# Performance work log

Measured on AMD Instinct MI355X. Metric: run time of the kernel, lower is better.

## Reference

```python
import jax, jax.numpy as jnp
import numpy as np

N_NODES = 50000
IN_CH = 32
HID = 64
N_EDGES = 800000
B = 4


def setup_inputs() -> dict:
    key = jax.random.key(0)
    ks = jax.random.split(key, 20)
    inp = {
        "x": jax.random.normal(ks[0], (B, N_NODES, IN_CH), dtype=jnp.float32),
        "h": jax.random.normal(ks[1], (B, N_NODES, HID), dtype=jnp.float32),
        "edge_index": jax.random.randint(ks[2], (2, N_EDGES), 0, N_NODES, dtype=jnp.int64),
        "edge_weight": jax.random.uniform(ks[3], (N_EDGES,), dtype=jnp.float32),
    }
    # 6 GCNConv layers: uz, hz, ur, hr, uh, hh. W stored as [in, out]; bias [out].
    names = [("uz", IN_CH), ("hz", HID), ("ur", IN_CH), ("hr", HID), ("uh", IN_CH), ("hh", HID)]
    for i, (nm, cin) in enumerate(names):
        scale = 1.0 / np.sqrt(cin)
        inp[f"W_{nm}"] = jax.random.uniform(ks[4 + 2 * i], (cin, HID), minval=-scale, maxval=scale, dtype=jnp.float32)
        inp[f"b_{nm}"] = jax.random.uniform(ks[5 + 2 * i], (HID,), minval=-scale, maxval=scale, dtype=jnp.float32)
    return inp


def _gcn_norm(edge_index, edge_weight, n):
    # add self-loops with weight 1, symmetric normalization (PyG GCNConv default)
    loop = jnp.arange(n, dtype=edge_index.dtype)
    src = jnp.concatenate([edge_index[0], loop])
    dst = jnp.concatenate([edge_index[1], loop])
    w = jnp.concatenate([edge_weight, jnp.ones((n,), edge_weight.dtype)])
    deg = jnp.zeros((n,), edge_weight.dtype).at[dst].add(w)
    dinv = jnp.where(deg > 0, jax.lax.rsqrt(jnp.maximum(deg, 1e-12)), 0.0)
    norm = dinv[src] * w * dinv[dst]
    return src, dst, norm


def _gcn(x, W, b, src, dst, norm, n):
    # x: [B, N, Cin] -> [B, N, H]; linear then normalized scatter-add over edges
    xw = jnp.einsum("bnc,ch->bnh", x, W)
    msg = xw[:, src, :] * norm[None, :, None]          # [B, E+N, H]
    agg = jnp.zeros((x.shape[0], n, W.shape[1]), x.dtype).at[:, dst].add(msg)
    return agg + b


def reference(x, h, edge_index, edge_weight,
              W_uz, b_uz, W_hz, b_hz, W_ur, b_ur, W_hr, b_hr, W_uh, b_uh, W_hh, b_hh):
    n = x.shape[1]
    src, dst, norm = _gcn_norm(edge_index, edge_weight, n)
    z = jax.nn.sigmoid(_gcn(x, W_uz, b_uz, src, dst, norm, n)
                       + _gcn(h, W_hz, b_hz, src, dst, norm, n))
    r = jax.nn.sigmoid(_gcn(x, W_ur, b_ur, src, dst, norm, n)
                       + _gcn(h, W_hr, b_hr, src, dst, norm, n))
    h_hat = jnp.tanh(_gcn(x, W_uh, b_uh, src, dst, norm, n)
                     + _gcn(r * h, W_hh, b_hh, src, dst, norm, n))
    return (1.0 - z) * h + z * h_hat
```

## Files before the change

### kernel.cpp

```cpp
#include <hip/hip_runtime.h>
#include <math.h>

#define NN 50000
#define CIN 32
#define HD  64
#define NE  800000
#define NB  4
#define NBLK 196
#define NTILE 12500
#define TPB   3125

typedef unsigned int uint32;
typedef unsigned short ushort16;
typedef __attribute__((ext_vector_type(8))) short bf16x8;
typedef __attribute__((ext_vector_type(4))) float f32x4;

__device__ __forceinline__ uint32 pk2(float a, float b) {
    uint32 ua = __float_as_uint(a), ub = __float_as_uint(b);
    uint32 ra = (ua + 0x7FFFu + ((ua >> 16) & 1u)) >> 16;
    uint32 rb = (ub + 0x7FFFu + ((ub >> 16) & 1u)) >> 16;
    return ra | (rb << 16);
}
__device__ __forceinline__ ushort16 b1(float v) {
    uint32 u = __float_as_uint(v);
    return (ushort16)((u + 0x7FFFu + ((u >> 16) & 1u)) >> 16);
}
__device__ __forceinline__ float blo(uint32 v) { return __uint_as_float(v << 16); }
__device__ __forceinline__ float bhi(uint32 v) { return __uint_as_float(v & 0xFFFF0000u); }
__device__ __forceinline__ float sigm(float v) { return 1.0f / (1.0f + __expf(-v)); }


__global__ void k_init(float* __restrict__ deg, int* __restrict__ counts) {
    int i = blockIdx.x * blockDim.x + threadIdx.x;
    if (i < NN) { deg[i] = 1.0f; counts[i] = 0; }
}

__global__ void k_deg_count(const int* __restrict__ ei, const float* __restrict__ ew,
                            float* __restrict__ deg, int* __restrict__ counts) {
    int stride = gridDim.x * blockDim.x;
    for (int e = blockIdx.x * blockDim.x + threadIdx.x; e < NE; e += stride) {
        int d = ei[NE + e];
        atomicAdd(&deg[d], ew[e]);
        atomicAdd(&counts[d], 1);
    }
}

__global__ void k_convert(const float* __restrict__ x, const float* __restrict__ h,
                          uint32* __restrict__ F) {
    int stride = gridDim.x * blockDim.x;
    for (int t = blockIdx.x * blockDim.x + threadIdx.x; t < NB * NN * (CIN / 2); t += stride) {
        int cp = t & 15; int rest = t >> 4;
        int b = rest / NN; int n = rest - b * NN;
        float2 v = *(const float2*)&x[(b * NN + n) * CIN + 2 * cp];
        F[n * 192 + b * 16 + cp] = pk2(v.x, v.y);
    }
    for (int t = blockIdx.x * blockDim.x + threadIdx.x; t < NB * NN * (HD / 2); t += stride) {
        int cp = t & 31; int rest = t >> 5;
        int b = rest / NN; int n = rest - b * NN;
        float2 v = *(const float2*)&h[(b * NN + n) * HD + 2 * cp];
        F[n * 192 + 64 + b * 32 + cp] = pk2(v.x, v.y);
    }
}

__global__ void k_pack(const float* __restrict__ Wuz, const float* __restrict__ Whz,
                       const float* __restrict__ Wur, const float* __restrict__ Whr,
                       const float* __restrict__ Wuh, const float* __restrict__ Whh,
                       const float* __restrict__ buz, const float* __restrict__ bhz,
                       const float* __restrict__ bur, const float* __restrict__ bhr,
                       const float* __restrict__ buh, const float* __restrict__ bhh,
                       uint32* __restrict__ WB, float* __restrict__ BS) {
    int t = blockIdx.x * blockDim.x + threadIdx.x;
    if (t < 9216) {
        int g = t / 3072, rem = t - g * 3072;
        int kt = rem >> 10, r2 = rem & 1023;
        int ct = r2 >> 8, r3 = r2 & 255;
        int l = r3 >> 2, jp = r3 & 3;
        int k = kt * 32 + ((l >> 4) << 3) + 2 * jp;
        int ch = ct * 16 + (l & 15);
        const float* Wu = (g == 0) ? Wuz : (g == 1) ? Wur : Wuh;
        const float* Wh = (g == 0) ? Whz : (g == 1) ? Whr : Whh;
        float w0 = (k < 32) ? Wu[k * 64 + ch] : Wh[(k - 32) * 64 + ch];
        int k1 = k + 1;
        float w1 = (k1 < 32) ? Wu[k1 * 64 + ch] : Wh[(k1 - 32) * 64 + ch];
        WB[t] = pk2(w0, w1);
    }
    if (t < 192) {
        int g = t >> 6, c = t & 63;
        const float* bu = (g == 0) ? buz : (g == 1) ? bur : buh;
        const float* bh = (g == 0) ? bhz : (g == 1) ? bhr : bhh;
        BS[t] = bu[c] + bh[c];
    }
}


__global__ void k_scan1(const int* __restrict__ counts, int* __restrict__ tmp,
                        int* __restrict__ partials) {
    __shared__ int lds[256];
    int i = blockIdx.x * 256 + threadIdx.x;
    int v = (i < NN) ? counts[i] : 0;
    lds[threadIdx.x] = v;
    __syncthreads();
    for (int off = 1; off < 256; off <<= 1) {
        int t = (threadIdx.x >= off) ? lds[threadIdx.x - off] : 0;
        __syncthreads();
        lds[threadIdx.x] += t;
        __syncthreads();
    }
    if (i < NN) tmp[i] = lds[threadIdx.x];
    if (threadIdx.x == 255) partials[blockIdx.x] = lds[255];
}

__global__ void k_scan2(int* __restrict__ partials) {
    __shared__ int lds[256];
    int v = (threadIdx.x < NBLK) ? partials[threadIdx.x] : 0;
    lds[threadIdx.x] = v;
    __syncthreads();
    for (int off = 1; off < 256; off <<= 1) {
        int t = (threadIdx.x >= off) ? lds[threadIdx.x - off] : 0;
        __syncthreads();
        lds[threadIdx.x] += t;
        __syncthreads();
    }
    int ex = (threadIdx.x > 0) ? lds[threadIdx.x - 1] : 0;
    if (threadIdx.x < NBLK) partials[threadIdx.x] = ex;
}

__global__ void k_scan3(const int* __restrict__ tmp, const int* __restrict__ counts,
                        const int* __restrict__ partials,
                        int* __restrict__ rowptr, int* __restrict__ cursor,
                        float* __restrict__ deg) {
    int i = blockIdx.x * blockDim.x + threadIdx.x;
    if (i < NN) {
        int inc = tmp[i] + partials[i >> 8];
        rowptr[i + 1] = inc;
        cursor[i] = inc - counts[i];
        if (i == 0) rowptr[0] = 0;
        float dg = deg[i];
        deg[i] = (dg > 0.0f) ? rsqrtf(fmaxf(dg, 1e-12f)) : 0.0f;
    }
}

__global__ void k_bucket(const int* __restrict__ ei, const float* __restrict__ ew,
                         const float* __restrict__ dinv,
                         int* __restrict__ cursor, int2* __restrict__ eb) {
    int stride = gridDim.x * blockDim.x;
    for (int e = blockIdx.x * blockDim.x + threadIdx.x; e < NE; e += stride) {
        int s = ei[e], d = ei[NE + e];
        float nrm = dinv[s] * ew[e] * dinv[d];
        int pos = atomicAdd(&cursor[d], 1);
        eb[pos] = make_int2(s, __float_as_int(nrm));
    }
}


__global__ __launch_bounds__(256) void k_gather_xh(
    const int* __restrict__ rowptr, const int2* __restrict__ eb,
    const float* __restrict__ dinv, const uint32* __restrict__ F,
    uint32* __restrict__ AggU) {

    int l = threadIdx.x & 63;
    int d = __builtin_amdgcn_readfirstlane(blockIdx.x * 4 + (threadIdx.x >> 6));
    float dv = dinv[d];
    float s2 = dv * dv;

    const uint32* fp = F + 3 * l;
    const uint32* sp = fp + d * 192;
    uint32 u0 = sp[0], u1 = sp[1], u2 = sp[2];
    float a0 = s2 * blo(u0), a1 = s2 * bhi(u0);
    float a2 = s2 * blo(u1), a3 = s2 * bhi(u1);
    float a4 = s2 * blo(u2), a5 = s2 * bhi(u2);

    int e  = rowptr[d];
    int e1 = rowptr[d + 1];

    for (; e + 3 < e1; e += 4) {
        int2 p0 = eb[e], p1 = eb[e + 1], p2 = eb[e + 2], p3 = eb[e + 3];
        const uint32* q0 = fp + p0.x * 192;
        const uint32* q1 = fp + p1.x * 192;
        const uint32* q2 = fp + p2.x * 192;
        const uint32* q3 = fp + p3.x * 192;
        uint32 v00 = q0[0], v01 = q0[1], v02 = q0[2];
        uint32 v10 = q1[0], v11 = q1[1], v12 = q1[2];
        uint32 v20 = q2[0], v21 = q2[1], v22 = q2[2];
        uint32 v30 = q3[0], v31 = q3[1], v32 = q3[2];
        float n0 = __int_as_float(p0.y), n1 = __int_as_float(p1.y);
        float n2 = __int_as_float(p2.y), n3 = __int_as_float(p3.y);
        a0 = fmaf(n0, blo(v00), a0); a1 = fmaf(n0, bhi(v00), a1);
        a2 = fmaf(n0, blo(v01), a2); a3 = fmaf(n0, bhi(v01), a3);
        a4 = fmaf(n0, blo(v02), a4); a5 = fmaf(n0, bhi(v02), a5);
        a0 = fmaf(n1, blo(v10), a0); a1 = fmaf(n1, bhi(v10), a1);
        a2 = fmaf(n1, blo(v11), a2); a3 = fmaf(n1, bhi(v11), a3);
        a4 = fmaf(n1, blo(v12), a4); a5 = fmaf(n1, bhi(v12), a5);
        a0 = fmaf(n2, blo(v20), a0); a1 = fmaf(n2, bhi(v20), a1);
        a2 = fmaf(n2, blo(v21), a2); a3 = fmaf(n2, bhi(v21), a3);
        a4 = fmaf(n2, blo(v22), a4); a5 = fmaf(n2, bhi(v22), a5);
        a0 = fmaf(n3, blo(v30), a0); a1 = fmaf(n3, bhi(v30), a1);
        a2 = fmaf(n3, blo(v31), a2); a3 = fmaf(n3, bhi(v31), a3);
        a4 = fmaf(n3, blo(v32), a4); a5 = fmaf(n3, bhi(v32), a5);
    }
    for (; e < e1; ++e) {
        int2 p0 = eb[e];
        const uint32* q0 = fp + p0.x * 192;
        uint32 v00 = q0[0], v01 = q0[1], v02 = q0[2];
        float n0 = __int_as_float(p0.y);
        a0 = fmaf(n0, blo(v00), a0); a1 = fmaf(n0, bhi(v00), a1);
        a2 = fmaf(n0, blo(v01), a2); a3 = fmaf(n0, bhi(v01), a3);
        a4 = fmaf(n0, blo(v02), a4); a5 = fmaf(n0, bhi(v02), a5);
    }

    uint32 w0 = pk2(a0, a1), w1 = pk2(a2, a3), w2 = pk2(a4, a5);
    int j = 3 * l;
    #pragma unroll
    for (int q = 0; q < 3; ++q) {
        uint32 wv = (q == 0) ? w0 : (q == 1) ? w1 : w2;
        int jq = j + q;
        int b, s;
        if (jq < 64) { b = jq >> 4; s = jq & 15; }
        else { int jj = jq - 64; b = jj >> 5; s = 16 + (jj & 31); }
        AggU[(b * NN + d) * 48 + s] = wv;
    }
}

__global__ __launch_bounds__(256) void k_gather_rh(
    const int* __restrict__ rowptr, const int2* __restrict__ eb,
    const float* __restrict__ dinv, const uint32* __restrict__ R,
    uint32* __restrict__ AggU) {

    int l = threadIdx.x & 63;
    int d = __builtin_amdgcn_readfirstlane(blockIdx.x * 4 + (threadIdx.x >> 6));
    float dv = dinv[d];
    float s2 = dv * dv;

    const uint32* rp = R + 2 * l;
    uint2 sv = *(const uint2*)(rp + d * 128);
    float a0 = s2 * blo(sv.x), a1 = s2 * bhi(sv.x);
    float a2 = s2 * blo(sv.y), a3 = s2 * bhi(sv.y);

    int e  = rowptr[d];
    int e1 = rowptr[d + 1];

    for (; e + 3 < e1; e += 4) {
        int2 p0 = eb[e], p1 = eb[e + 1], p2 = eb[e + 2], p3 = eb[e + 3];
        uint2 v0 = *(const uint2*)(rp + p0.x * 128);
        uint2 v1 = *(const uint2*)(rp + p1.x * 128);
        uint2 v2 = *(const uint2*)(rp + p2.x * 128);
        uint2 v3 = *(const uint2*)(rp + p3.x * 128);
        float n0 = __int_as_float(p0.y), n1 = __int_as_float(p1.y);
        float n2 = __int_as_float(p2.y), n3 = __int_as_float(p3.y);
        a0 = fmaf(n0, blo(v0.x), a0); a1 = fmaf(n0, bhi(v0.x), a1);
        a2 = fmaf(n0, blo(v0.y), a2); a3 = fmaf(n0, bhi(v0.y), a3);
        a0 = fmaf(n1, blo(v1.x), a0); a1 = fmaf(n1, bhi(v1.x), a1);
        a2 = fmaf(n1, blo(v1.y), a2); a3 = fmaf(n1, bhi(v1.y), a3);
        a0 = fmaf(n2, blo(v2.x), a0); a1 = fmaf(n2, bhi(v2.x), a1);
        a2 = fmaf(n2, blo(v2.y), a2); a3 = fmaf(n2, bhi(v2.y), a3);
        a0 = fmaf(n3, blo(v3.x), a0); a1 = fmaf(n3, bhi(v3.x), a1);
        a2 = fmaf(n3, blo(v3.y), a2); a3 = fmaf(n3, bhi(v3.y), a3);
    }
    for (; e < e1; ++e) {
        int2 p0 = eb[e];
        uint2 v0 = *(const uint2*)(rp + p0.x * 128);
        float n0 = __int_as_float(p0.y);
        a0 = fmaf(n0, blo(v0.x), a0); a1 = fmaf(n0, bhi(v0.x), a1);
        a2 = fmaf(n0, blo(v0.y), a2); a3 = fmaf(n0, bhi(v0.y), a3);
    }

    int b  = l >> 4;
    int cp = (2 * l) & 31;
    *(uint2*)&AggU[(b * NN + d) * 48 + 16 + cp] = make_uint2(pk2(a0, a1), pk2(a2, a3));
}


__global__ __launch_bounds__(256) void k_zr(
    const uint32* __restrict__ AggU, const float* __restrict__ h,
    const uint32* __restrict__ WB, const float* __restrict__ BS,
    float* __restrict__ z_out, ushort16* __restrict__ R16) {

    int l  = threadIdx.x & 63;
    int t  = blockIdx.x * 4 + (threadIdx.x >> 6);
    int lr = l & 15, lg = l >> 4;

    const bf16x8* wz = (const bf16x8*)WB;
    const bf16x8* wr = (const bf16x8*)(WB + 3072);
    const bf16x8* arow = (const bf16x8*)(AggU + (t * 16 + lr) * 48);
    bf16x8 af0 = arow[0 * 4 + lg];
    bf16x8 af1 = arow[1 * 4 + lg];
    bf16x8 af2 = arow[2 * 4 + lg];

    f32x4 az[4], ar[4];
    #pragma unroll
    for (int c = 0; c < 4; ++c) { az[c] = (f32x4){0,0,0,0}; ar[c] = (f32x4){0,0,0,0}; }

    #pragma unroll
    for (int ct = 0; ct < 4; ++ct) {
        az[ct] = __builtin_amdgcn_mfma_f32_16x16x32_bf16(af0, wz[(0*4+ct)*64 + l], az[ct], 0,0,0);
        ar[ct] = __builtin_amdgcn_mfma_f32_16x16x32_bf16(af0, wr[(0*4+ct)*64 + l], ar[ct], 0,0,0);
        az[ct] = __builtin_amdgcn_mfma_f32_16x16x32_bf16(af1, wz[(1*4+ct)*64 + l], az[ct], 0,0,0);
        ar[ct] = __builtin_amdgcn_mfma_f32_16x16x32_bf16(af1, wr[(1*4+ct)*64 + l], ar[ct], 0,0,0);
        az[ct] = __builtin_amdgcn_mfma_f32_16x16x32_bf16(af2, wz[(2*4+ct)*64 + l], az[ct], 0,0,0);
        ar[ct] = __builtin_amdgcn_mfma_f32_16x16x32_bf16(af2, wr[(2*4+ct)*64 + l], ar[ct], 0,0,0);
    }

    int bb    = t / TPB;
    int pr0   = t * 16;
    int nbase = pr0 - bb * NN;

    #pragma unroll
    for (int ct = 0; ct < 4; ++ct) {
        int ch = ct * 16 + lr;
        float bz = BS[ch];
        float br = BS[64 + ch];
        #pragma unroll
        for (int rr = 0; rr < 4; ++rr) {
            int i    = lg * 4 + rr;
            int off  = (pr0 + i) * 64 + ch;
            float zv = sigm(az[ct][rr] + bz);
            float rv = sigm(ar[ct][rr] + br);
            float hv = h[off];
            z_out[off] = zv;
            R16[(nbase + i) * 256 + bb * 64 + ch] = b1(rv * hv);
        }
    }
}

__global__ __launch_bounds__(256) void k_final(
    const uint32* __restrict__ AggU, const float* __restrict__ h,
    const uint32* __restrict__ WB, const float* __restrict__ BS,
    float* __restrict__ out) {

    int l  = threadIdx.x & 63;
    int t  = blockIdx.x * 4 + (threadIdx.x >> 6);
    int lr = l & 15, lg = l >> 4;

    const bf16x8* wh = (const bf16x8*)(WB + 6144);
    const bf16x8* arow = (const bf16x8*)(AggU + (t * 16 + lr) * 48);
    bf16x8 af0 = arow[0 * 4 + lg];
    bf16x8 af1 = arow[1 * 4 + lg];
    bf16x8 af2 = arow[2 * 4 + lg];

    f32x4 ac[4];
    #pragma unroll
    for (int c = 0; c < 4; ++c) ac[c] = (f32x4){0,0,0,0};

    #pragma unroll
    for (int ct = 0; ct < 4; ++ct) {
        ac[ct] = __builtin_amdgcn_mfma_f32_16x16x32_bf16(af0, wh[(0*4+ct)*64 + l], ac[ct], 0,0,0);
        ac[ct] = __builtin_amdgcn_mfma_f32_16x16x32_bf16(af1, wh[(1*4+ct)*64 + l], ac[ct], 0,0,0);
        ac[ct] = __builtin_amdgcn_mfma_f32_16x16x32_bf16(af2, wh[(2*4+ct)*64 + l], ac[ct], 0,0,0);
    }

    int pr0 = t * 16;

    #pragma unroll
    for (int ct = 0; ct < 4; ++ct) {
        int ch = ct * 16 + lr;
        float bs = BS[128 + ch];
        #pragma unroll
        for (int rr = 0; rr < 4; ++rr) {
            int i   = lg * 4 + rr;
            int off = (pr0 + i) * 64 + ch;
            float hh = tanhf(ac[ct][rr] + bs);
            float zv = out[off];
            float hv = h[off];
            out[off] = (1.0f - zv) * hv + zv * hh;
        }
    }
}


extern "C" void kernel_launch(void* const* d_in, const int* in_sizes, int n_in,
                              void* d_out, int out_size, void* d_ws, size_t ws_size,
                              hipStream_t stream) {
    const float* x   = (const float*)d_in[0];
    const float* h   = (const float*)d_in[1];
    const int*   ei  = (const int*)d_in[2];
    const float* ew  = (const float*)d_in[3];
    const float* Wuz = (const float*)d_in[4];
    const float* buz = (const float*)d_in[5];
    const float* Whz = (const float*)d_in[6];
    const float* bhz = (const float*)d_in[7];
    const float* Wur = (const float*)d_in[8];
    const float* bur = (const float*)d_in[9];
    const float* Whr = (const float*)d_in[10];
    const float* bhr = (const float*)d_in[11];
    const float* Wuh = (const float*)d_in[12];
    const float* buh = (const float*)d_in[13];
    const float* Whh = (const float*)d_in[14];
    const float* bhh = (const float*)d_in[15];
    float* out = (float*)d_out;

    float*  w      = (float*)d_ws;
    float*  dinv   = w;
    int*    rowptr = (int*)(w + 51200);
    int2*   eb     = (int2*)(w + 102400);
    uint32* F      = (uint32*)(w + 1702400);
    uint32* R      = F;
    uint32* AggU   = (uint32*)(w + 11302400);
    uint32* WB     = (uint32*)(w + 20902400);
    float*  BS     = (float*)(w + 20911616);
    int*    counts = (int*)(w + 20911808);
    int*    tmp    = (int*)(w + 20963008);
    int*    cursor = (int*)(w + 21014208);
    int*    parts  = (int*)(w + 21065408);

    k_init<<<(NN + 255) / 256, 256, 0, stream>>>(dinv, counts);
    k_deg_count<<<2048, 256, 0, stream>>>(ei, ew, dinv, counts);
    k_convert<<<2048, 256, 0, stream>>>(x, h, F);
    k_pack<<<36, 256, 0, stream>>>(Wuz, Whz, Wur, Whr, Wuh, Whh,
                                   buz, bhz, bur, bhr, buh, bhh, WB, BS);

    k_scan1<<<NBLK, 256, 0, stream>>>(counts, tmp, parts);
    k_scan2<<<1, 256, 0, stream>>>(parts);
    k_scan3<<<NBLK, 256, 0, stream>>>(tmp, counts, parts, rowptr, cursor, dinv);

    k_bucket<<<2048, 256, 0, stream>>>(ei, ew, dinv, cursor, eb);

    k_gather_xh<<<NN / 4, 256, 0, stream>>>(rowptr, eb, dinv, F, AggU);

    k_zr<<<NTILE / 4, 256, 0, stream>>>(AggU, h, WB, BS, out, (ushort16*)R);

    k_gather_rh<<<NN / 4, 256, 0, stream>>>(rowptr, eb, dinv, R, AggU);

    k_final<<<NTILE / 4, 256, 0, stream>>>(AggU, h, WB, BS, out);
}
```

Baseline: 367.9 us.

## Fuse preprocessing kernels, unroll gathers by 8, persist MFMA weights in registers

Merges degree counting, feature conversion and weight packing into one launch. Both gather kernels get an 8-edge unrolled loop for more loads in flight, and the aggregated buffer switches to a node-major 192-word row layout with contiguous stores. The zr and final kernels become grid-stride over tiles with a fixed wave count and keep their weight fragments and biases in registers. This trades launch and weight-reload cost for higher register pressure and a different store pattern.

Result: slower. 381.7 us (+3.8%).

```diff
diff --git a/kernel.cpp b/kernel.cpp
--- a/kernel.cpp
+++ b/kernel.cpp
@@ -9,9 +9,10 @@
 #define NBLK 196
 #define NTILE 12500
 #define TPB   3125
+#define DWAVES 2048
 
 typedef unsigned int uint32;
-typedef unsigned short ushort16;
+typedef unsigned short ushort_t;
 typedef __attribute__((ext_vector_type(8))) short bf16x8;
 typedef __attribute__((ext_vector_type(4))) float f32x4;
 
@@ -21,9 +22,9 @@
     uint32 rb = (ub + 0x7FFFu + ((ub >> 16) & 1u)) >> 16;
     return ra | (rb << 16);
 }
-__device__ __forceinline__ ushort16 b1(float v) {
+__device__ __forceinline__ ushort_t b1(float v) {
     uint32 u = __float_as_uint(v);
-    return (ushort16)((u + 0x7FFFu + ((u >> 16) & 1u)) >> 16);
+    return (ushort_t)((u + 0x7FFFu + ((u >> 16) & 1u)) >> 16);
 }
 __device__ __forceinline__ float blo(uint32 v) { return __uint_as_float(v << 16); }
 __device__ __forceinline__ float bhi(uint32 v) { return __uint_as_float(v & 0xFFFF0000u); }
@@ -35,43 +36,22 @@
     if (i < NN) { deg[i] = 1.0f; counts[i] = 0; }
 }
 
-__global__ void k_deg_count(const int* __restrict__ ei, const float* __restrict__ ew,
-                            float* __restrict__ deg, int* __restrict__ counts) {
+__global__ void k_pre(const float* __restrict__ x, const float* __restrict__ h,
+                      const int* __restrict__ ei, const float* __restrict__ ew,
+                      const float* __restrict__ Wuz, const float* __restrict__ Whz,
+                      const float* __restrict__ Wur, const float* __restrict__ Whr,
+                      const float* __restrict__ Wuh, const float* __restrict__ Whh,
+                      const float* __restrict__ buz, const float* __restrict__ bhz,
+                      const float* __restrict__ bur, const float* __restrict__ bhr,
+                      const float* __restrict__ buh, const float* __restrict__ bhh,
+                      uint32* __restrict__ F, float* __restrict__ deg,
+                      int* __restrict__ counts,
+                      uint32* __restrict__ WB, float* __restrict__ BS) {
     int stride = gridDim.x * blockDim.x;
-    for (int e = blockIdx.x * blockDim.x + threadIdx.x; e < NE; e += stride) {
-        int d = ei[NE + e];
-        atomicAdd(&deg[d], ew[e]);
-        atomicAdd(&counts[d], 1);
-    }
-}
-
-__global__ void k_convert(const float* __restrict__ x, const float* __restrict__ h,
-                          uint32* __restrict__ F) {
-    int stride = gridDim.x * blockDim.x;
-    for (int t = blockIdx.x * blockDim.x + threadIdx.x; t < NB * NN * (CIN / 2); t += stride) {
-        int cp = t & 15; int rest = t >> 4;
-        int b = rest / NN; int n = rest - b * NN;
-        float2 v = *(const float2*)&x[(b * NN + n) * CIN + 2 * cp];
-        F[n * 192 + b * 16 + cp] = pk2(v.x, v.y);
-    }
-    for (int t = blockIdx.x * blockDim.x + threadIdx.x; t < NB * NN * (HD / 2); t += stride) {
-        int cp = t & 31; int rest = t >> 5;
-        int b = rest / NN; int n = rest - b * NN;
-        float2 v = *(const float2*)&h[(b * NN + n) * HD + 2 * cp];
-        F[n * 192 + 64 + b * 32 + cp] = pk2(v.x, v.y);
-    }
-}
-
-__global__ void k_pack(const float* __restrict__ Wuz, const float* __restrict__ Whz,
-                       const float* __restrict__ Wur, const float* __restrict__ Whr,
-                       const float* __restrict__ Wuh, const float* __restrict__ Whh,
-                       const float* __restrict__ buz, const float* __restrict__ bhz,
-                       const float* __restrict__ bur, const float* __restrict__ bhr,
-                       const float* __restrict__ buh, const float* __restrict__ bhh,
-                       uint32* __restrict__ WB, float* __restrict__ BS) {
-    int t = blockIdx.x * blockDim.x + threadIdx.x;
-    if (t < 9216) {
-        int g = t / 3072, rem = t - g * 3072;
+    int tid = blockIdx.x * blockDim.x + threadIdx.x;
+
+    if (tid < 9216) {
+        int g = tid / 3072, rem = tid - g * 3072;
         int kt = rem >> 10, r2 = rem & 1023;
         int ct = r2 >> 8, r3 = r2 & 255;
         int l = r3 >> 2, jp = r3 & 3;
@@ -82,13 +62,31 @@
         float w0 = (k < 32) ? Wu[k * 64 + ch] : Wh[(k - 32) * 64 + ch];
         int k1 = k + 1;
         float w1 = (k1 < 32) ? Wu[k1 * 64 + ch] : Wh[(k1 - 32) * 64 + ch];
-        WB[t] = pk2(w0, w1);
-    }
-    if (t < 192) {
-        int g = t >> 6, c = t & 63;
+        WB[tid] = pk2(w0, w1);
+    }
+    if (tid < 192) {
+        int g = tid >> 6, c = tid & 63;
         const float* bu = (g == 0) ? buz : (g == 1) ? bur : buh;
         const float* bh = (g == 0) ? bhz : (g == 1) ? bhr : bhh;
-        BS[t] = bu[c] + bh[c];
+        BS[tid] = bu[c] + bh[c];
+    }
+
+    for (int t = tid; t < NB * NN * (CIN / 2); t += stride) {
+        int cp = t & 15; int rest = t >> 4;
+        int b = rest / NN; int n = rest - b * NN;
+        float2 v = *(const float2*)&x[(b * NN + n) * CIN + 2 * cp];
+        F[n * 192 + b * 16 + cp] = pk2(v.x, v.y);
+    }
+    for (int t = tid; t < NB * NN * (HD / 2); t += stride) {
+        int cp = t & 31; int rest = t >> 5;
+        int b = rest / NN; int n = rest - b * NN;
+        float2 v = *(const float2*)&h[(b * NN + n) * HD + 2 * cp];
+        F[n * 192 + 64 + b * 32 + cp] = pk2(v.x, v.y);
+    }
+    for (int e = tid; e < NE; e += stride) {
+        int d = ei[NE + e];
+        atomicAdd(&deg[d], ew[e]);
+        atomicAdd(&counts[d], 1);
     }
 }
 
@@ -173,6 +171,54 @@
     int e  = rowptr[d];
     int e1 = rowptr[d + 1];
 
+    for (; e + 7 < e1; e += 8) {
+        int2 p0 = eb[e],     p1 = eb[e + 1], p2 = eb[e + 2], p3 = eb[e + 3];
+        int2 p4 = eb[e + 4], p5 = eb[e + 5], p6 = eb[e + 6], p7 = eb[e + 7];
+        const uint32* q0 = fp + p0.x * 192;
+        const uint32* q1 = fp + p1.x * 192;
+        const uint32* q2 = fp + p2.x * 192;
+        const uint32* q3 = fp + p3.x * 192;
+        const uint32* q4 = fp + p4.x * 192;
+        const uint32* q5 = fp + p5.x * 192;
+        const uint32* q6 = fp + p6.x * 192;
+        const uint32* q7 = fp + p7.x * 192;
+        uint32 v00 = q0[0], v01 = q0[1], v02 = q0[2];
+        uint32 v10 = q1[0], v11 = q1[1], v12 = q1[2];
+        uint32 v20 = q2[0], v21 = q2[1], v22 = q2[2];
+        uint32 v30 = q3[0], v31 = q3[1], v32 = q3[2];
+        uint32 v40 = q4[0], v41 = q4[1], v42 = q4[2];
+        uint32 v50 = q5[0], v51 = q5[1], v52 = q5[2];
+        uint32 v60 = q6[0], v61 = q6[1], v62 = q6[2];
+        uint32 v70 = q7[0], v71 = q7[1], v72 = q7[2];
+        float n0 = __int_as_float(p0.y), n1 = __int_as_float(p1.y);
+        float n2 = __int_as_float(p2.y), n3 = __int_as_float(p3.y);
+        float n4 = __int_as_float(p4.y), n5 = __int_as_float(p5.y);
+        float n6 = __int_as_float(p6.y), n7 = __int_as_float(p7.y);
+        a0 = fmaf(n0, blo(v00), a0); a1 = fmaf(n0, bhi(v00), a1);
+        a2 = fmaf(n0, blo(v01), a2); a3 = fmaf(n0, bhi(v01), a3);
+        a4 = fmaf(n0, blo(v02), a4); a5 = fmaf(n0, bhi(v02), a5);
+        a0 = fmaf(n1, blo(v10), a0); a1 = fmaf(n1, bhi(v10), a1);
+        a2 = fmaf(n1, blo(v11), a2); a3 = fmaf(n1, bhi(v11), a3);
+        a4 = fmaf(n1, blo(v12), a4); a5 = fmaf(n1, bhi(v12), a5);
+        a0 = fmaf(n2, blo(v20), a0); a1 = fmaf(n2, bhi(v20), a1);
+        a2 = fmaf(n2, blo(v21), a2); a3 = fmaf(n2, bhi(v21), a3);
+        a4 = fmaf(n2, blo(v22), a4); a5 = fmaf(n2, bhi(v22), a5);
+        a0 = fmaf(n3, blo(v30), a0); a1 = fmaf(n3, bhi(v30), a1);
+        a2 = fmaf(n3, blo(v31), a2); a3 = fmaf(n3, bhi(v31), a3);
+        a4 = fmaf(n3, blo(v32), a4); a5 = fmaf(n3, bhi(v32), a5);
+        a0 = fmaf(n4, blo(v40), a0); a1 = fmaf(n4, bhi(v40), a1);
+        a2 = fmaf(n4, blo(v41), a2); a3 = fmaf(n4, bhi(v41), a3);
+        a4 = fmaf(n4, blo(v42), a4); a5 = fmaf(n4, bhi(v42), a5);
+        a0 = fmaf(n5, blo(v50), a0); a1 = fmaf(n5, bhi(v50), a1);
+        a2 = fmaf(n5, blo(v51), a2); a3 = fmaf(n5, bhi(v51), a3);
+        a4 = fmaf(n5, blo(v52), a4); a5 = fmaf(n5, bhi(v52), a5);
+        a0 = fmaf(n6, blo(v60), a0); a1 = fmaf(n6, bhi(v60), a1);
+        a2 = fmaf(n6, blo(v61), a2); a3 = fmaf(n6, bhi(v61), a3);
+        a4 = fmaf(n6, blo(v62), a4); a5 = fmaf(n6, bhi(v62), a5);
+        a0 = fmaf(n7, blo(v70), a0); a1 = fmaf(n7, bhi(v70), a1);
+        a2 = fmaf(n7, blo(v71), a2); a3 = fmaf(n7, bhi(v71), a3);
+        a4 = fmaf(n7, blo(v72), a4); a5 = fmaf(n7, bhi(v72), a5);
+    }
     for (; e + 3 < e1; e += 4) {
         int2 p0 = eb[e], p1 = eb[e + 1], p2 = eb[e + 2], p3 = eb[e + 3];
         const uint32* q0 = fp + p0.x * 192;
@@ -208,17 +254,10 @@
         a4 = fmaf(n0, blo(v02), a4); a5 = fmaf(n0, bhi(v02), a5);
     }
 
-    uint32 w0 = pk2(a0, a1), w1 = pk2(a2, a3), w2 = pk2(a4, a5);
-    int j = 3 * l;
-    #pragma unroll
-    for (int q = 0; q < 3; ++q) {
-        uint32 wv = (q == 0) ? w0 : (q == 1) ? w1 : w2;
-        int jq = j + q;
-        int b, s;
-        if (jq < 64) { b = jq >> 4; s = jq & 15; }
-        else { int jj = jq - 64; b = jj >> 5; s = 16 + (jj & 31); }
-        AggU[(b * NN + d) * 48 + s] = wv;
-    }
+    uint32* op = AggU + d * 192 + 3 * l;
+    op[0] = pk2(a0, a1);
+    op[1] = pk2(a2, a3);
+    op[2] = pk2(a4, a5);
 }
 
 __global__ __launch_bounds__(256) void k_gather_rh(
@@ -239,6 +278,38 @@
     int e  = rowptr[d];
     int e1 = rowptr[d + 1];
 
+    for (; e + 7 < e1; e += 8) {
+        int2 p0 = eb[e],     p1 = eb[e + 1], p2 = eb[e + 2], p3 = eb[e + 3];
+        int2 p4 = eb[e + 4], p5 = eb[e + 5], p6 = eb[e + 6], p7 = eb[e + 7];
+        uint2 v0 = *(const uint2*)(rp + p0.x * 128);
+        uint2 v1 = *(const uint2*)(rp + p1.x * 128);
+        uint2 v2 = *(const uint2*)(rp + p2.x * 128);
+        uint2 v3 = *(const uint2*)(rp + p3.x * 128);
+        uint2 v4 = *(const uint2*)(rp + p4.x * 128);
+        uint2 v5 = *(const uint2*)(rp + p5.x * 128);
+        uint2 v6 = *(const uint2*)(rp + p6.x * 128);
+        uint2 v7 = *(const uint2*)(rp + p7.x * 128);
+        float n0 = __int_as_float(p0.y), n1 = __int_as_float(p1.y);
+        float n2 = __int_as_float(p2.y), n3 = __int_as_float(p3.y);
+        float n4 = __int_as_float(p4.y), n5 = __int_as_float(p5.y);
+        float n6 = __int_as_float(p6.y), n7 = __int_as_float(p7.y);
+        a0 = fmaf(n0, blo(v0.x), a0); a1 = fmaf(n0, bhi(v0.x), a1);
+        a2 = fmaf(n0, blo(v0.y), a2); a3 = fmaf(n0, bhi(v0.y), a3);
+        a0 = fmaf(n1, blo(v1.x), a0); a1 = fmaf(n1, bhi(v1.x), a1);
+        a2 = fmaf(n1, blo(v1.y), a2); a3 = fmaf(n1, bhi(v1.y), a3);
+        a0 = fmaf(n2, blo(v2.x), a0); a1 = fmaf(n2, bhi(v2.x), a1);
+        a2 = fmaf(n2, blo(v2.y), a2); a3 = fmaf(n2, bhi(v2.y), a3);
+        a0 = fmaf(n3, blo(v3.x), a0); a1 = fmaf(n3, bhi(v3.x), a1);
+        a2 = fmaf(n3, blo(v3.y), a2); a3 = fmaf(n3, bhi(v3.y), a3);
+        a0 = fmaf(n4, blo(v4.x), a0); a1 = fmaf(n4, bhi(v4.x), a1);
+        a2 = fmaf(n4, blo(v4.y), a2); a3 = fmaf(n4, bhi(v4.y), a3);
+        a0 = fmaf(n5, blo(v5.x), a0); a1 = fmaf(n5, bhi(v5.x), a1);
+        a2 = fmaf(n5, blo(v5.y), a2); a3 = fmaf(n5, bhi(v5.y), a3);
+        a0 = fmaf(n6, blo(v6.x), a0); a1 = fmaf(n6, bhi(v6.x), a1);
+        a2 = fmaf(n6, blo(v6.y), a2); a3 = fmaf(n6, bhi(v6.y), a3);
+        a0 = fmaf(n7, blo(v7.x), a0); a1 = fmaf(n7, bhi(v7.x), a1);
+        a2 = fmaf(n7, blo(v7.y), a2); a3 = fmaf(n7, bhi(v7.y), a3);
+    }
     for (; e + 3 < e1; e += 4) {
         int2 p0 = eb[e], p1 = eb[e + 1], p2 = eb[e + 2], p3 = eb[e + 3];
         uint2 v0 = *(const uint2*)(rp + p0.x * 128);
@@ -264,60 +335,67 @@
         a2 = fmaf(n0, blo(v0.y), a2); a3 = fmaf(n0, bhi(v0.y), a3);
     }
 
-    int b  = l >> 4;
-    int cp = (2 * l) & 31;
-    *(uint2*)&AggU[(b * NN + d) * 48 + 16 + cp] = make_uint2(pk2(a0, a1), pk2(a2, a3));
+    *(uint2*)&AggU[d * 192 + 64 + (l >> 4) * 32 + ((2 * l) & 31)] =
+        make_uint2(pk2(a0, a1), pk2(a2, a3));
 }
 
 
 __global__ __launch_bounds__(256) void k_zr(
     const uint32* __restrict__ AggU, const float* __restrict__ h,
     const uint32* __restrict__ WB, const float* __restrict__ BS,
-    float* __restrict__ z_out, ushort16* __restrict__ R16) {
+    float* __restrict__ z_out, ushort_t* __restrict__ R16) {
 
     int l  = threadIdx.x & 63;
-    int t  = blockIdx.x * 4 + (threadIdx.x >> 6);
+    int wv = blockIdx.x * 4 + (threadIdx.x >> 6);
     int lr = l & 15, lg = l >> 4;
 
     const bf16x8* wz = (const bf16x8*)WB;
     const bf16x8* wr = (const bf16x8*)(WB + 3072);
-    const bf16x8* arow = (const bf16x8*)(AggU + (t * 16 + lr) * 48);
-    bf16x8 af0 = arow[0 * 4 + lg];
-    bf16x8 af1 = arow[1 * 4 + lg];
-    bf16x8 af2 = arow[2 * 4 + lg];
-
-    f32x4 az[4], ar[4];
+    bf16x8 wzf[12], wrf[12];
     #pragma unroll
-    for (int c = 0; c < 4; ++c) { az[c] = (f32x4){0,0,0,0}; ar[c] = (f32x4){0,0,0,0}; }
-
+    for (int f = 0; f < 12; ++f) { wzf[f] = wz[f * 64 + l]; wrf[f] = wr[f * 64 + l]; }
+    float bz[4], br[4];
     #pragma unroll
     for (int ct = 0; ct < 4; ++ct) {
-        az[ct] = __builtin_amdgcn_mfma_f32_16x16x32_bf16(af0, wz[(0*4+ct)*64 + l], az[ct], 0,0,0);
-        ar[ct] = __builtin_amdgcn_mfma_f32_16x16x32_bf16(af0, wr[(0*4+ct)*64 + l], ar[ct], 0,0,0);
-        az[ct] = __builtin_amdgcn_mfma_f32_16x16x32_bf16(af1, wz[(1*4+ct)*64 + l], az[ct], 0,0,0);
-        ar[ct] = __builtin_amdgcn_mfma_f32_16x16x32_bf16(af1, wr[(1*4+ct)*64 + l], ar[ct], 0,0,0);
-        az[ct] = __builtin_amdgcn_mfma_f32_16x16x32_bf16(af2, wz[(2*4+ct)*64 + l], az[ct], 0,0,0);
-        ar[ct] = __builtin_amdgcn_mfma_f32_16x16x32_bf16(af2, wr[(2*4+ct)*64 + l], ar[ct], 0,0,0);
-    }
-
-    int bb    = t / TPB;
-    int pr0   = t * 16;
-    int nbase = pr0 - bb * NN;
-
-    #pragma unroll
-    for (int ct = 0; ct < 4; ++ct) {
-        int ch = ct * 16 + lr;
-        float bz = BS[ch];
-        float br = BS[64 + ch];
+        bz[ct] = BS[ct * 16 + lr];
+        br[ct] = BS[64 + ct * 16 + lr];
+    }
+
+    for (int t = wv; t < NTILE; t += DWAVES) {
+        int bb = t / TPB, nt = t - bb * TPB;
+        const uint32* base = AggU + (nt * 16 + lr) * 192;
+        bf16x8 af0 = *(const bf16x8*)(base + bb * 16 + lg * 4);
+        bf16x8 af1 = *(const bf16x8*)(base + 64 + bb * 32 + lg * 4);
+        bf16x8 af2 = *(const bf16x8*)(base + 64 + bb * 32 + 16 + lg * 4);
+
+        f32x4 az[4], ar[4];
         #pragma unroll
-        for (int rr = 0; rr < 4; ++rr) {
-            int i    = lg * 4 + rr;
-            int off  = (pr0 + i) * 64 + ch;
-            float zv = sigm(az[ct][rr] + bz);
-            float rv = sigm(ar[ct][rr] + br);
-            float hv = h[off];
-            z_out[off] = zv;
-            R16[(nbase + i) * 256 + bb * 64 + ch] = b1(rv * hv);
+        for (int c = 0; c < 4; ++c) { az[c] = (f32x4){0,0,0,0}; ar[c] = (f32x4){0,0,0,0}; }
+
+        #pragma unroll
+        for (int ct = 0; ct < 4; ++ct) {
+            az[ct] = __builtin_amdgcn_mfma_f32_16x16x32_bf16(af0, wzf[0*4+ct], az[ct], 0,0,0);
+            ar[ct] = __builtin_amdgcn_mfma_f32_16x16x32_bf16(af0, wrf[0*4+ct], ar[ct], 0,0,0);
+            az[ct] = __builtin_amdgcn_mfma_f32_16x16x32_bf16(af1, wzf[1*4+ct], az[ct], 0,0,0);
+            ar[ct] = __builtin_amdgcn_mfma_f32_16x16x32_bf16(af1, wrf[1*4+ct], ar[ct], 0,0,0);
+            az[ct] = __builtin_amdgcn_mfma_f32_16x16x32_bf16(af2, wzf[2*4+ct], az[ct], 0,0,0);
+            ar[ct] = __builtin_amdgcn_mfma_f32_16x16x32_bf16(af2, wrf[2*4+ct], ar[ct], 0,0,0);
+        }
+
+        int node0 = nt * 16;
+        #pragma unroll
+        for (int ct = 0; ct < 4; ++ct) {
+            int ch = ct * 16 + lr;
+            #pragma unroll
+            for (int rr = 0; rr < 4; ++rr) {
+                int node = node0 + lg * 4 + rr;
+                int off  = (bb * NN + node) * 64 + ch;
+                float zv = sigm(az[ct][rr] + bz[ct]);
+                float rv = sigm(ar[ct][rr] + br[ct]);
+                float hv = h[off];
+                z_out[off] = zv;
+                R16[node * 256 + bb * 64 + ch] = b1(rv * hv);
+            }
         }
     }
 }
@@ -328,40 +406,48 @@
     float* __restrict__ out) {
 
     int l  = threadIdx.x & 63;
-    int t  = blockIdx.x * 4 + (threadIdx.x >> 6);
+    int wv = blockIdx.x * 4 + (threadIdx.x >> 6);
     int lr = l & 15, lg = l >> 4;
 
     const bf16x8* wh = (const bf16x8*)(WB + 6144);
-    const bf16x8* arow = (const bf16x8*)(AggU + (t * 16 + lr) * 48);
-    bf16x8 af0 = arow[0 * 4 + lg];
-    bf16x8 af1 = arow[1 * 4 + lg];
-    bf16x8 af2 = arow[2 * 4 + lg];
-
-    f32x4 ac[4];
+    bf16x8 whf[12];
     #pragma unroll
-    for (int c = 0; c < 4; ++c) ac[c] = (f32x4){0,0,0,0};
-
+    for (int f = 0; f < 12; ++f) whf[f] = wh[f * 64 + l];
+    float bs[4];
     #pragma unroll
-    for (int ct = 0; ct < 4; ++ct) {
-        ac[ct] = __builtin_amdgcn_mfma_f32_16x16x32_bf16(af0, wh[(0*4+ct)*64 + l], ac[ct], 0,0,0);
-        ac[ct] = __builtin_amdgcn_mfma_f32_16x16x32_bf16(af1, wh[(1*4+ct)*64 + l], ac[ct], 0,0,0);
-        ac[ct] = __builtin_amdgcn_mfma_f32_16x16x32_bf16(af2, wh[(2*4+ct)*64 + l], ac[ct], 0,0,0);
-    }
-
-    int pr0 = t * 16;
-
-    #pragma unroll
-    for (int ct = 0; ct < 4; ++ct) {
-        int ch = ct * 16 + lr;
-        float bs = BS[128 + ch];
+    for (int ct = 0; ct < 4; ++ct) bs[ct] = BS[128 + ct * 16 + lr];
+
+    for (int t = wv; t < NTILE; t += DWAVES) {
+        int bb = t / TPB, nt = t - bb * TPB;
+        const uint32* base = AggU + (nt * 16 + lr) * 192;
+        bf16x8 af0 = *(const bf16x8*)(base + bb * 16 + lg * 4);
+        bf16x8 af1 = *(const bf16x8*)(base + 64 + bb * 32 + lg * 4);
+        bf16x8 af2 = *(const bf16x8*)(base + 64 + bb * 32 + 16 + lg * 4);
+
+        f32x4 ac[4];
         #pragma unroll
-        for (int rr = 0; rr < 4; ++rr) {
-            int i   = lg * 4 + rr;
-            int off = (pr0 + i) * 64 + ch;
-            float hh = tanhf(ac[ct][rr] + bs);
-            float zv = out[off];
-            float hv = h[off];
-            out[off] = (1.0f - zv) * hv + zv * hh;
+        for (int c = 0; c < 4; ++c) ac[c] = (f32x4){0,0,0,0};
+
+        #pragma unroll
+        for (int ct = 0; ct < 4; ++ct) {
+            ac[ct] = __builtin_amdgcn_mfma_f32_16x16x32_bf16(af0, whf[0*4+ct], ac[ct], 0,0,0);
+            ac[ct] = __builtin_amdgcn_mfma_f32_16x16x32_bf16(af1, whf[1*4+ct], ac[ct], 0,0,0);
+            ac[ct] = __builtin_amdgcn_mfma_f32_16x16x32_bf16(af2, whf[2*4+ct], ac[ct], 0,0,0);
+        }
+
+        int node0 = nt * 16;
+        #pragma unroll
+        for (int ct = 0; ct < 4; ++ct) {
+            int ch = ct * 16 + lr;
+            #pragma unroll
+            for (int rr = 0; rr < 4; ++rr) {
+                int node = node0 + lg * 4 + rr;
+                int off  = (bb * NN + node) * 64 + ch;
+                float hh = tanhf(ac[ct][rr] + bs[ct]);
+                float zv = out[off];
+                float hv = h[off];
+                out[off] = (1.0f - zv) * hv + zv * hh;
+            }
         }
     }
 }
@@ -403,10 +489,10 @@
     int*    parts  = (int*)(w + 21065408);
 
     k_init<<<(NN + 255) / 256, 256, 0, stream>>>(dinv, counts);
-    k_deg_count<<<2048, 256, 0, stream>>>(ei, ew, dinv, counts);
-    k_convert<<<2048, 256, 0, stream>>>(x, h, F);
-    k_pack<<<36, 256, 0, stream>>>(Wuz, Whz, Wur, Whr, Wuh, Whh,
-                                   buz, bhz, bur, bhr, buh, bhh, WB, BS);
+    k_pre<<<2048, 256, 0, stream>>>(x, h, ei, ew,
+                                    Wuz, Whz, Wur, Whr, Wuh, Whh,
+                                    buz, bhz, bur, bhr, buh, bhh,
+                                    F, dinv, counts, WB, BS);
 
     k_scan1<<<NBLK, 256, 0, stream>>>(counts, tmp, parts);
     k_scan2<<<1, 256, 0, stream>>>(parts);
@@ -416,9 +502,9 @@
 
     k_gather_xh<<<NN / 4, 256, 0, stream>>>(rowptr, eb, dinv, F, AggU);
 
-    k_zr<<<NTILE / 4, 256, 0, stream>>>(AggU, h, WB, BS, out, (ushort16*)R);
+    k_zr<<<DWAVES / 4, 256, 0, stream>>>(AggU, h, WB, BS, out, (ushort_t*)R);
 
     k_gather_rh<<<NN / 4, 256, 0, stream>>>(rowptr, eb, dinv, R, AggU);
 
-    k_final<<<NTILE / 4, 256, 0, stream>>>(AggU, h, WB, BS, out);
-}
+    k_final<<<DWAVES / 4, 256, 0, stream>>>(AggU, h, WB, BS, out);
+}
```
